# Performance work log

Measured on AMD Instinct MI355X. Metric: run time of the kernel, lower is better.

The kernel has to match this reference:

```python
import jax, jax.numpy as jnp
import numpy as np

B, L, D = 32, 4096, 64
TOP_K = 2
KS = 25            # AvgPool1d kernel_size
PAD = (KS - 1) // 2
LN_EPS = 1e-5


def setup_inputs() -> dict:
    key = jax.random.key(0)
    ks = jax.random.split(key, 8)
    s = lambda fan_in: 1.0 / np.sqrt(fan_in)
    return {
        "x": jax.random.normal(ks[0], (B, L, 1), dtype=jnp.float32),
        "embed_w": jax.random.normal(ks[1], (1, D), dtype=jnp.float32) * s(1),
        "embed_b": jnp.zeros((D,), jnp.float32),
        "q_w": jax.random.normal(ks[2], (D, D), dtype=jnp.float32) * s(D),
        "q_b": jnp.zeros((D,), jnp.float32),
        "k_w": jax.random.normal(ks[3], (D, D), dtype=jnp.float32) * s(D),
        "k_b": jnp.zeros((D,), jnp.float32),
        "v_w": jax.random.normal(ks[4], (D, D), dtype=jnp.float32) * s(D),
        "v_b": jnp.zeros((D,), jnp.float32),
        "ln_g": jnp.ones((D,), jnp.float32),
        "ln_b": jnp.zeros((D,), jnp.float32),
        "fc_w": jax.random.normal(ks[5], (L * D, 1), dtype=jnp.float32) * s(L * D),
        "fc_b": jnp.zeros((1,), jnp.float32),
    }


def _auto_correlation(h, q_w, q_b, k_w, k_b, v_w, v_b):
    Q = h @ q_w + q_b          # (B, L, D)
    K = h @ k_w + k_b
    V = h @ v_w + v_b
    q_fft = jnp.fft.rfft(Q, axis=1)
    k_fft = jnp.fft.rfft(K, axis=1)
    corr = jnp.fft.irfft(q_fft * jnp.conj(k_fft), n=L, axis=1)  # (B, L, D)
    mean_corr = corr.mean(axis=-1)                               # (B, L)
    topk_vals, topk_idx = jax.lax.top_k(mean_corr, TOP_K)        # (B, K)
    weights = jax.nn.softmax(topk_vals, axis=-1)                 # (B, K)
    # torch.roll(V[b], shift=lag): out[i] = V[(i - lag) mod L]
    idx = (jnp.arange(L)[None, None, :] - topk_idx[:, :, None]) % L   # (B, K, L)
    Vg = jnp.take_along_axis(V[:, None, :, :], idx[..., None], axis=2)  # (B, K, L, D)
    return jnp.einsum("bk,bkld->bld", weights, Vg)


def _moving_avg(h):
    # AvgPool1d(kernel=KS, stride=1, pad=PAD, count_include_pad=True) over time axis
    hp = jnp.pad(h, ((0, 0), (PAD, PAD), (0, 0)))
    cs = jnp.pad(jnp.cumsum(hp, axis=1), ((0, 0), (1, 0), (0, 0)))
    return (cs[:, KS:, :] - cs[:, :-KS, :]) / KS   # (B, L, D)


def reference(x, embed_w, embed_b, q_w, q_b, k_w, k_b, v_w, v_b,
              ln_g, ln_b, fc_w, fc_b):
    h = x @ embed_w + embed_b                       # (B, L, D)
    ac = _auto_correlation(h, q_w, q_b, k_w, k_b, v_w, v_b)
    z = h + ac
    mu = z.mean(axis=-1, keepdims=True)
    var = z.var(axis=-1, keepdims=True)
    hn = (z - mu) * jax.lax.rsqrt(var + LN_EPS) * ln_g + ln_b
    trend = _moving_avg(hn)
    seasonal = hn - trend
    return seasonal.reshape(B, L * D) @ fc_w + fc_b  # (B, 1)
```

## Files before the change

### kernel.cpp

```cpp
#include <hip/hip_runtime.h>
#include <math.h>

#define LQ 4096
#define DQ 64
#define BQ 32
#define KSQ 25
#define PADQ 12
#define LN_EPS 1e-5f

#define NT 8
#define TCH (LQ / NT)

#define WS_U    16
#define WS_V    80
#define WS_W    144
#define WS_F    256
#define WS_TOP  (WS_F + 4 * LQ)
#define WS_PART (WS_TOP + BQ * 4)

__device__ __forceinline__ float wave_sum64(float v) {
    for (int o = 32; o > 0; o >>= 1) v += __shfl_xor(v, o, 64);
    return v;
}

__global__ void ac_prep_kernel(const float* __restrict__ embed_w,
                               const float* __restrict__ embed_b,
                               const float* __restrict__ q_w, const float* __restrict__ q_b,
                               const float* __restrict__ k_w, const float* __restrict__ k_b,
                               const float* __restrict__ v_w, const float* __restrict__ v_b,
                               const float* __restrict__ ln_g,
                               float* __restrict__ ws) {
    int d = threadIdx.x;
    float Aq = 0.f, Cq = 0.f, Ak = 0.f, Ck = 0.f, Av = 0.f, Cv = 0.f;
#pragma unroll 8
    for (int e = 0; e < DQ; ++e) {
        float we = embed_w[e], be = embed_b[e];
        float qw = q_w[e * DQ + d], kw = k_w[e * DQ + d], vw = v_w[e * DQ + d];
        Aq = fmaf(we, qw, Aq); Cq = fmaf(be, qw, Cq);
        Ak = fmaf(we, kw, Ak); Ck = fmaf(be, kw, Ck);
        Av = fmaf(we, vw, Av); Cv = fmaf(be, vw, Cv);
    }
    Cq += q_b[d]; Ck += k_b[d]; Cv += v_b[d];

    float cx = embed_w[d];
    float cs = Av;
    float cc = embed_b[d] + Cv;

    const float invD = 1.f / (float)DQ;
    float mx = wave_sum64(cx) * invD;
    float ms = wave_sum64(cs) * invD;
    float mc = wave_sum64(cc) * invD;
    float cxp = cx - mx, csp = cs - ms, ccp = cc - mc;

    float Mxx = wave_sum64(cxp * cxp) * invD;
    float Mss = wave_sum64(csp * csp) * invD;
    float Mcc = wave_sum64(ccp * ccp) * invD;
    float Mxs = wave_sum64(cxp * csp) * invD;
    float Mxc = wave_sum64(cxp * ccp) * invD;
    float Msc = wave_sum64(csp * ccp) * invD;

    float alpha = wave_sum64(Aq * Ak) * invD;
    float beta  = wave_sum64(Aq * Ck + Ak * Cq) * invD;
    float gamma = wave_sum64(Cq * Ck) * ((float)LQ * invD);

    float g = ln_g[d];
    ws[WS_U + d] = cxp * g;
    ws[WS_V + d] = csp * g;
    ws[WS_W + d] = ccp * g;
    if (d == 0) {
        ws[0] = alpha; ws[1] = beta; ws[2] = gamma;
        ws[3] = Mxx; ws[4] = Mss; ws[5] = Mcc;
        ws[6] = Mxs; ws[7] = Mxc; ws[8] = Msc;
    }
}

__global__ void ac_prepF_kernel(const float* __restrict__ fc_w,
                                const float* __restrict__ ln_b,
                                float* __restrict__ ws) {
    __shared__ float su[DQ], sv[DQ], sw[DQ], sb[DQ];
    if (threadIdx.x < DQ) {
        su[threadIdx.x] = ws[WS_U + threadIdx.x];
        sv[threadIdx.x] = ws[WS_V + threadIdx.x];
        sw[threadIdx.x] = ws[WS_W + threadIdx.x];
        sb[threadIdx.x] = ln_b[threadIdx.x];
    }
    __syncthreads();
    int l = blockIdx.x * 256 + threadIdx.x;
    const float4* fc = (const float4*)(fc_w + (size_t)l * DQ);
    float fu = 0.f, fv = 0.f, fw = 0.f, fb = 0.f;
#pragma unroll
    for (int d4 = 0; d4 < DQ / 4; ++d4) {
        float4 f = fc[d4];
        int d = d4 * 4;
        fu = fmaf(su[d], f.x, fu); fu = fmaf(su[d+1], f.y, fu); fu = fmaf(su[d+2], f.z, fu); fu = fmaf(su[d+3], f.w, fu);
        fv = fmaf(sv[d], f.x, fv); fv = fmaf(sv[d+1], f.y, fv); fv = fmaf(sv[d+2], f.z, fv); fv = fmaf(sv[d+3], f.w, fv);
        fw = fmaf(sw[d], f.x, fw); fw = fmaf(sw[d+1], f.y, fw); fw = fmaf(sw[d+2], f.z, fw); fw = fmaf(sw[d+3], f.w, fw);
        fb = fmaf(sb[d], f.x, fb); fb = fmaf(sb[d+1], f.y, fb); fb = fmaf(sb[d+2], f.z, fb); fb = fmaf(sb[d+3], f.w, fb);
    }
    ws[WS_F + l]          = fu;
    ws[WS_F + LQ + l]     = fv;
    ws[WS_F + 2 * LQ + l] = fw;
    ws[WS_F + 3 * LQ + l] = fb;
}

__global__ void ac_autocorr_kernel(const float* __restrict__ x,
                                   float* __restrict__ ws) {
    __shared__ float sA[TCH];
    __shared__ float sB[TCH + 1024];
    int b = blockIdx.x;
    int lagbase = blockIdx.y << 10;
    int t0 = blockIdx.z * TCH;
    const float* xb = x + (size_t)b * LQ;
    int tid = threadIdx.x;

    for (int i = tid; i < TCH; i += 256) sA[i] = xb[t0 + i];
    int start = t0 - lagbase - 1023;
    for (int j = tid; j < TCH + 1024; j += 256)
        sB[j] = xb[(start + j + LQ) & (LQ - 1)];
    __syncthreads();

    const float4* sA4 = (const float4*)sA;
    const float4* sB4 = (const float4*)sB;
    int base = 255 - tid;
    float4 w0 = sB4[base];
    float a0 = 0.f, a1 = 0.f, a2 = 0.f, a3 = 0.f;
#pragma unroll 4
    for (int c = 0; c < TCH / 4; ++c) {
        float4 w1 = sB4[base + c + 1];
        float4 xa = sA4[c];
        a0 = fmaf(xa.x, w0.w, a0); a1 = fmaf(xa.x, w0.z, a1); a2 = fmaf(xa.x, w0.y, a2); a3 = fmaf(xa.x, w0.x, a3);
        a0 = fmaf(xa.y, w1.x, a0); a1 = fmaf(xa.y, w0.w, a1); a2 = fmaf(xa.y, w0.z, a2); a3 = fmaf(xa.y, w0.y, a3);
        a0 = fmaf(xa.z, w1.y, a0); a1 = fmaf(xa.z, w1.x, a1); a2 = fmaf(xa.z, w0.w, a2); a3 = fmaf(xa.z, w0.z, a3);
        a0 = fmaf(xa.w, w1.z, a0); a1 = fmaf(xa.w, w1.y, a1); a2 = fmaf(xa.w, w1.x, a2); a3 = fmaf(xa.w, w0.w, a3);
        w0 = w1;
    }
    float4* part4 = (float4*)(ws + WS_PART);
    part4[((size_t)(blockIdx.z * BQ + b) * 512) + (blockIdx.y * 256) + tid] =
        make_float4(a0, a1, a2, a3);
}

__device__ __forceinline__ bool ac_better(float v, int i, float v2, int i2) {
    return (v > v2) || (v == v2 && i < i2);
}
__global__ void ac_top2_kernel(const float* __restrict__ x,
                               float* __restrict__ ws) {
    __shared__ float sred[256], rred[256];
    __shared__ float sv0[256], sv1[256];
    __shared__ int   si0[256], si1[256];
    int b = blockIdx.x;
    int tid = threadIdx.x;
    const float* xb = x + (size_t)b * LQ;

    float sx = 0.f, r2k = 0.f;
    for (int t = tid; t < LQ; t += 256) {
        float v = xb[t];
        sx  += v;
        r2k += v * xb[(t + 2048) & (LQ - 1)];
    }
    sred[tid] = sx; rred[tid] = r2k;
    __syncthreads();
    for (int st = 128; st > 0; st >>= 1) {
        if (tid < st) { sred[tid] += sred[tid + st]; rred[tid] += rred[tid + st]; }
        __syncthreads();
    }
    float Sx = sred[0], R2048 = rred[0];
    float alpha = ws[0], beta = ws[1], gamma = ws[2];
    float cbase = fmaf(beta, Sx, gamma);

    float v0 = -3.0e38f, v1 = -3.0e38f;
    int i0 = 1 << 30, i1 = 1 << 30;
    const float* part = ws + WS_PART;
    for (int lag = tid; lag < 2048; lag += 256) {
        float R = 0.f;
#pragma unroll
        for (int z = 0; z < NT; ++z)
            R += part[((size_t)(z * BQ + b) * 2048) + lag];
        float v = fmaf(alpha, R, cbase);
        if (ac_better(v, lag, v0, i0)) { v1 = v0; i1 = i0; v0 = v; i0 = lag; }
        else if (ac_better(v, lag, v1, i1)) { v1 = v; i1 = lag; }
        int mir = (LQ - lag) & (LQ - 1);
        if (mir != lag) {
            if (ac_better(v, mir, v0, i0)) { v1 = v0; i1 = i0; v0 = v; i0 = mir; }
            else if (ac_better(v, mir, v1, i1)) { v1 = v; i1 = mir; }
        }
    }
    if (tid == 0) {
        float v = fmaf(alpha, R2048, cbase);
        if (ac_better(v, 2048, v0, i0)) { v1 = v0; i1 = i0; v0 = v; i0 = 2048; }
        else if (ac_better(v, 2048, v1, i1)) { v1 = v; i1 = 2048; }
    }
    sv0[tid] = v0; sv1[tid] = v1; si0[tid] = i0; si1[tid] = i1;
    __syncthreads();
    for (int st = 128; st > 0; st >>= 1) {
        if (tid < st) {
            float a0 = sv0[tid], a1 = sv1[tid];
            int   c0 = si0[tid], c1 = si1[tid];
            float u0 = sv0[tid + st], u1 = sv1[tid + st];
            int   j0 = si0[tid + st], j1 = si1[tid + st];
            float t0v, t1v; int t0i, t1i;
            if (ac_better(a0, c0, u0, j0)) {
                t0v = a0; t0i = c0;
                if (ac_better(u0, j0, a1, c1)) { t1v = u0; t1i = j0; } else { t1v = a1; t1i = c1; }
            } else {
                t0v = u0; t0i = j0;
                if (ac_better(a0, c0, u1, j1)) { t1v = a0; t1i = c0; } else { t1v = u1; t1i = j1; }
            }
            sv0[tid] = t0v; si0[tid] = t0i;
            sv1[tid] = t1v; si1[tid] = t1i;
        }
        __syncthreads();
    }
    if (tid == 0) {
        float w0 = 1.f / (1.f + expf(sv1[0] - sv0[0]));
        float* top = ws + WS_TOP + b * 4;
        top[0] = (float)si0[0]; top[1] = (float)si1[0];
        top[2] = w0; top[3] = 1.f - w0;
    }
}

__global__ void ac_final_kernel(const float* __restrict__ x,
                                const float* __restrict__ fc_b,
                                const float* __restrict__ ws,
                                float* __restrict__ out) {
    __shared__ float pL[LQ], qL[LQ], rL[LQ];
    __shared__ float wred[16];
    int b = blockIdx.x;
    int tid = threadIdx.x;
    const float* xb = x + (size_t)b * LQ;
    const float* top = ws + WS_TOP + b * 4;
    int lag0 = (int)top[0], lag1 = (int)top[1];
    float w0 = top[2], w1 = top[3];
    float Mxx = ws[3], Mss = ws[4], Mcc = ws[5], Mxs = ws[6], Mxc = ws[7], Msc = ws[8];

    for (int l = tid; l < LQ; l += 1024) {
        float xv = xb[l];
        float xs = w0 * xb[(l - lag0) & (LQ - 1)] + w1 * xb[(l - lag1) & (LQ - 1)];
        float var = xv * xv * Mxx + xs * xs * Mss + Mcc
                  + 2.f * xv * xs * Mxs + 2.f * xv * Mxc + 2.f * xs * Msc;
        float r = rsqrtf(var + LN_EPS);
        pL[l] = xv * r; qL[l] = xs * r; rL[l] = r;
    }
    __syncthreads();

    const float* Fu = ws + WS_F;
    const float* Fv = Fu + LQ;
    const float* Fw = Fv + LQ;
    const float* FB = Fw + LQ;
    const float inv = 1.f / (float)KSQ;
    float acc = 0.f;
    for (int l = tid; l < LQ; l += 1024) {
        int lo = l - PADQ; if (lo < 0) lo = 0;
        int hi = l + PADQ; if (hi > LQ - 1) hi = LQ - 1;
        float sp = 0.f, sq = 0.f, sr = 0.f;
        for (int j = lo; j <= hi; ++j) { sp += pL[j]; sq += qL[j]; sr += rL[j]; }
        float cnt = (float)(hi - lo + 1);
        acc += (pL[l] - sp * inv) * Fu[l]
             + (qL[l] - sq * inv) * Fv[l]
             + (rL[l] - sr * inv) * Fw[l]
             + (1.f - cnt * inv) * FB[l];
    }
    acc = wave_sum64(acc);
    int wid = tid >> 6;
    if ((tid & 63) == 0) wred[wid] = acc;
    __syncthreads();
    if (tid == 0) {
        float s = 0.f;
#pragma unroll
        for (int w = 0; w < 16; ++w) s += wred[w];
        out[b] = s + fc_b[0];
    }
}

extern "C" void kernel_launch(void* const* d_in, const int* in_sizes, int n_in,
                              void* d_out, int out_size, void* d_ws, size_t ws_size,
                              hipStream_t stream) {
    const float* x       = (const float*)d_in[0];
    const float* embed_w = (const float*)d_in[1];
    const float* embed_b = (const float*)d_in[2];
    const float* q_w     = (const float*)d_in[3];
    const float* q_b     = (const float*)d_in[4];
    const float* k_w     = (const float*)d_in[5];
    const float* k_b     = (const float*)d_in[6];
    const float* v_w     = (const float*)d_in[7];
    const float* v_b     = (const float*)d_in[8];
    const float* ln_g    = (const float*)d_in[9];
    const float* ln_b    = (const float*)d_in[10];
    const float* fc_w    = (const float*)d_in[11];
    const float* fc_b    = (const float*)d_in[12];
    float* out = (float*)d_out;
    float* ws  = (float*)d_ws;

    ac_prep_kernel<<<1, 64, 0, stream>>>(embed_w, embed_b, q_w, q_b, k_w, k_b,
                                         v_w, v_b, ln_g, ws);
    ac_prepF_kernel<<<16, 256, 0, stream>>>(fc_w, ln_b, ws);
    ac_autocorr_kernel<<<dim3(BQ, 2, NT), 256, 0, stream>>>(x, ws);
    ac_top2_kernel<<<BQ, 256, 0, stream>>>(x, ws);
    ac_final_kernel<<<BQ, 1024, 0, stream>>>(x, fc_b, ws, out);
}
```

Measured before the change: 128.4 us.

## Fuse five kernels into two and move moving-average onto fc weights

Merges the parameter prep, fc-weight projection and autocorrelation partial sums into one heterogeneous launch, and folds top-2 selection into the final kernel with wave-shuffle reductions. The moving-average subtraction is moved algebraically onto the projected fc weights (the pool is applied to the F vectors instead of the per-batch normalized signals), removing the 25-tap windowed loop per batch. This cuts launch count and per-batch work, at the cost of every final block redundantly recomputing the small prep scalars.

New measurement: 116.6 us. 9.2% less time.

```diff
diff --git a/kernel.cpp b/kernel.cpp
--- a/kernel.cpp
+++ b/kernel.cpp
@@ -10,263 +10,306 @@
 
 #define NT 8
 #define TCH (LQ / NT)
-
-#define WS_U    16
-#define WS_V    80
-#define WS_W    144
-#define WS_F    256
-#define WS_TOP  (WS_F + 4 * LQ)
-#define WS_PART (WS_TOP + BQ * 4)
+#define NAC (BQ * 2 * NT)
+
+#define WS_PART 16384
 
 __device__ __forceinline__ float wave_sum64(float v) {
     for (int o = 32; o > 0; o >>= 1) v += __shfl_xor(v, o, 64);
     return v;
 }
 
-__global__ void ac_prep_kernel(const float* __restrict__ embed_w,
-                               const float* __restrict__ embed_b,
-                               const float* __restrict__ q_w, const float* __restrict__ q_b,
-                               const float* __restrict__ k_w, const float* __restrict__ k_b,
-                               const float* __restrict__ v_w, const float* __restrict__ v_b,
-                               const float* __restrict__ ln_g,
-                               float* __restrict__ ws) {
-    int d = threadIdx.x;
-    float Aq = 0.f, Cq = 0.f, Ak = 0.f, Ck = 0.f, Av = 0.f, Cv = 0.f;
-#pragma unroll 8
-    for (int e = 0; e < DQ; ++e) {
-        float we = embed_w[e], be = embed_b[e];
-        float qw = q_w[e * DQ + d], kw = k_w[e * DQ + d], vw = v_w[e * DQ + d];
-        Aq = fmaf(we, qw, Aq); Cq = fmaf(be, qw, Cq);
-        Ak = fmaf(we, kw, Ak); Ck = fmaf(be, kw, Ck);
-        Av = fmaf(we, vw, Av); Cv = fmaf(be, vw, Cv);
-    }
-    Cq += q_b[d]; Ck += k_b[d]; Cv += v_b[d];
-
-    float cx = embed_w[d];
-    float cs = Av;
-    float cc = embed_b[d] + Cv;
-
-    const float invD = 1.f / (float)DQ;
-    float mx = wave_sum64(cx) * invD;
-    float ms = wave_sum64(cs) * invD;
-    float mc = wave_sum64(cc) * invD;
-    float cxp = cx - mx, csp = cs - ms, ccp = cc - mc;
-
-    float Mxx = wave_sum64(cxp * cxp) * invD;
-    float Mss = wave_sum64(csp * csp) * invD;
-    float Mcc = wave_sum64(ccp * ccp) * invD;
-    float Mxs = wave_sum64(cxp * csp) * invD;
-    float Mxc = wave_sum64(cxp * ccp) * invD;
-    float Msc = wave_sum64(csp * ccp) * invD;
-
-    float alpha = wave_sum64(Aq * Ak) * invD;
-    float beta  = wave_sum64(Aq * Ck + Ak * Cq) * invD;
-    float gamma = wave_sum64(Cq * Ck) * ((float)LQ * invD);
-
-    float g = ln_g[d];
-    ws[WS_U + d] = cxp * g;
-    ws[WS_V + d] = csp * g;
-    ws[WS_W + d] = ccp * g;
-    if (d == 0) {
-        ws[0] = alpha; ws[1] = beta; ws[2] = gamma;
-        ws[3] = Mxx; ws[4] = Mss; ws[5] = Mcc;
-        ws[6] = Mxs; ws[7] = Mxc; ws[8] = Msc;
-    }
-}
-
-__global__ void ac_prepF_kernel(const float* __restrict__ fc_w,
-                                const float* __restrict__ ln_b,
-                                float* __restrict__ ws) {
-    __shared__ float su[DQ], sv[DQ], sw[DQ], sb[DQ];
-    if (threadIdx.x < DQ) {
-        su[threadIdx.x] = ws[WS_U + threadIdx.x];
-        sv[threadIdx.x] = ws[WS_V + threadIdx.x];
-        sw[threadIdx.x] = ws[WS_W + threadIdx.x];
-        sb[threadIdx.x] = ln_b[threadIdx.x];
-    }
-    __syncthreads();
-    int l = blockIdx.x * 256 + threadIdx.x;
-    const float4* fc = (const float4*)(fc_w + (size_t)l * DQ);
-    float fu = 0.f, fv = 0.f, fw = 0.f, fb = 0.f;
-#pragma unroll
-    for (int d4 = 0; d4 < DQ / 4; ++d4) {
-        float4 f = fc[d4];
-        int d = d4 * 4;
-        fu = fmaf(su[d], f.x, fu); fu = fmaf(su[d+1], f.y, fu); fu = fmaf(su[d+2], f.z, fu); fu = fmaf(su[d+3], f.w, fu);
-        fv = fmaf(sv[d], f.x, fv); fv = fmaf(sv[d+1], f.y, fv); fv = fmaf(sv[d+2], f.z, fv); fv = fmaf(sv[d+3], f.w, fv);
-        fw = fmaf(sw[d], f.x, fw); fw = fmaf(sw[d+1], f.y, fw); fw = fmaf(sw[d+2], f.z, fw); fw = fmaf(sw[d+3], f.w, fw);
-        fb = fmaf(sb[d], f.x, fb); fb = fmaf(sb[d+1], f.y, fb); fb = fmaf(sb[d+2], f.z, fb); fb = fmaf(sb[d+3], f.w, fb);
-    }
-    ws[WS_F + l]          = fu;
-    ws[WS_F + LQ + l]     = fv;
-    ws[WS_F + 2 * LQ + l] = fw;
-    ws[WS_F + 3 * LQ + l] = fb;
-}
-
-__global__ void ac_autocorr_kernel(const float* __restrict__ x,
-                                   float* __restrict__ ws) {
-    __shared__ float sA[TCH];
-    __shared__ float sB[TCH + 1024];
-    int b = blockIdx.x;
-    int lagbase = blockIdx.y << 10;
-    int t0 = blockIdx.z * TCH;
-    const float* xb = x + (size_t)b * LQ;
-    int tid = threadIdx.x;
-
-    for (int i = tid; i < TCH; i += 256) sA[i] = xb[t0 + i];
-    int start = t0 - lagbase - 1023;
-    for (int j = tid; j < TCH + 1024; j += 256)
-        sB[j] = xb[(start + j + LQ) & (LQ - 1)];
-    __syncthreads();
-
-    const float4* sA4 = (const float4*)sA;
-    const float4* sB4 = (const float4*)sB;
-    int base = 255 - tid;
-    float4 w0 = sB4[base];
-    float a0 = 0.f, a1 = 0.f, a2 = 0.f, a3 = 0.f;
-#pragma unroll 4
-    for (int c = 0; c < TCH / 4; ++c) {
-        float4 w1 = sB4[base + c + 1];
-        float4 xa = sA4[c];
-        a0 = fmaf(xa.x, w0.w, a0); a1 = fmaf(xa.x, w0.z, a1); a2 = fmaf(xa.x, w0.y, a2); a3 = fmaf(xa.x, w0.x, a3);
-        a0 = fmaf(xa.y, w1.x, a0); a1 = fmaf(xa.y, w0.w, a1); a2 = fmaf(xa.y, w0.z, a2); a3 = fmaf(xa.y, w0.y, a3);
-        a0 = fmaf(xa.z, w1.y, a0); a1 = fmaf(xa.z, w1.x, a1); a2 = fmaf(xa.z, w0.w, a2); a3 = fmaf(xa.z, w0.z, a3);
-        a0 = fmaf(xa.w, w1.z, a0); a1 = fmaf(xa.w, w1.y, a1); a2 = fmaf(xa.w, w1.x, a2); a3 = fmaf(xa.w, w0.w, a3);
-        w0 = w1;
-    }
-    float4* part4 = (float4*)(ws + WS_PART);
-    part4[((size_t)(blockIdx.z * BQ + b) * 512) + (blockIdx.y * 256) + tid] =
-        make_float4(a0, a1, a2, a3);
-}
-
 __device__ __forceinline__ bool ac_better(float v, int i, float v2, int i2) {
     return (v > v2) || (v == v2 && i < i2);
 }
-__global__ void ac_top2_kernel(const float* __restrict__ x,
-                               float* __restrict__ ws) {
-    __shared__ float sred[256], rred[256];
-    __shared__ float sv0[256], sv1[256];
-    __shared__ int   si0[256], si1[256];
+
+__global__ void ac_stage1_kernel(const float* __restrict__ x,
+                                 const float* __restrict__ fc_w,
+                                 const float* __restrict__ ln_g,
+                                 const float* __restrict__ ln_b,
+                                 const float* __restrict__ embed_w,
+                                 const float* __restrict__ embed_b,
+                                 const float* __restrict__ v_w,
+                                 const float* __restrict__ v_b,
+                                 float* __restrict__ ws) {
+    __shared__ float smem[2048];
+    int tid = threadIdx.x;
+
+    if (blockIdx.x < NAC) {
+        float* sA = smem;
+        float* sB = smem + TCH;
+        int b = blockIdx.x & 31;
+        int y = (blockIdx.x >> 5) & 1;
+        int z = blockIdx.x >> 6;
+        int lagbase = y << 10;
+        int t0 = z * TCH;
+        const float* xb = x + (size_t)b * LQ;
+
+        for (int i = tid; i < TCH; i += 256) sA[i] = xb[t0 + i];
+        int start = t0 - lagbase - 1023;
+        for (int j = tid; j < TCH + 1024; j += 256)
+            sB[j] = xb[(start + j + LQ) & (LQ - 1)];
+        __syncthreads();
+
+        const float4* sA4 = (const float4*)sA;
+        const float4* sB4 = (const float4*)sB;
+        int base = 255 - tid;
+        float4 w0 = sB4[base];
+        float a0 = 0.f, a1 = 0.f, a2 = 0.f, a3 = 0.f;
+#pragma unroll 4
+        for (int c = 0; c < TCH / 4; ++c) {
+            float4 w1 = sB4[base + c + 1];
+            float4 xa = sA4[c];
+            a0 = fmaf(xa.x, w0.w, a0); a1 = fmaf(xa.x, w0.z, a1); a2 = fmaf(xa.x, w0.y, a2); a3 = fmaf(xa.x, w0.x, a3);
+            a0 = fmaf(xa.y, w1.x, a0); a1 = fmaf(xa.y, w0.w, a1); a2 = fmaf(xa.y, w0.z, a2); a3 = fmaf(xa.y, w0.y, a3);
+            a0 = fmaf(xa.z, w1.y, a0); a1 = fmaf(xa.z, w1.x, a1); a2 = fmaf(xa.z, w0.w, a2); a3 = fmaf(xa.z, w0.z, a3);
+            a0 = fmaf(xa.w, w1.z, a0); a1 = fmaf(xa.w, w1.y, a1); a2 = fmaf(xa.w, w1.x, a2); a3 = fmaf(xa.w, w0.w, a3);
+            w0 = w1;
+        }
+        float4* part4 = (float4*)(ws + WS_PART);
+        part4[((size_t)(z * BQ + b) * 512) + (y * 256) + tid] =
+            make_float4(a0, a1, a2, a3);
+    } else {
+        float* Hu = smem;
+        float* Hv = smem + 280;
+        float* Hw = smem + 560;
+        float* Hb = smem + 840;
+        float* su = smem + 1120;
+        float* sv = smem + 1184;
+        float* sw = smem + 1248;
+        float* sb = smem + 1312;
+
+        if (tid < DQ) {
+            int d = tid;
+            float Av = 0.f, Cv = 0.f;
+#pragma unroll 8
+            for (int e = 0; e < DQ; ++e) {
+                float vw = v_w[e * DQ + d];
+                Av = fmaf(embed_w[e], vw, Av);
+                Cv = fmaf(embed_b[e], vw, Cv);
+            }
+            Cv += v_b[d];
+            float cx = embed_w[d];
+            float cs = Av;
+            float cc = embed_b[d] + Cv;
+            const float invD = 1.f / (float)DQ;
+            float mx = wave_sum64(cx) * invD;
+            float ms = wave_sum64(cs) * invD;
+            float mc = wave_sum64(cc) * invD;
+            float g = ln_g[d];
+            su[d] = (cx - mx) * g;
+            sv[d] = (cs - ms) * g;
+            sw[d] = (cc - mc) * g;
+            sb[d] = ln_b[d];
+        }
+        __syncthreads();
+
+        int lbase = (blockIdx.x - NAC) * 256;
+        for (int i = tid; i < 256 + 2 * PADQ; i += 256) {
+            int l = lbase - PADQ + i;
+            float fu = 0.f, fv = 0.f, fw = 0.f, fb = 0.f;
+            if (l >= 0 && l < LQ) {
+                const float4* fc = (const float4*)(fc_w + (size_t)l * DQ);
+#pragma unroll
+                for (int d4 = 0; d4 < DQ / 4; ++d4) {
+                    float4 f = fc[d4];
+                    int d = d4 * 4;
+                    fu = fmaf(su[d], f.x, fu); fu = fmaf(su[d+1], f.y, fu); fu = fmaf(su[d+2], f.z, fu); fu = fmaf(su[d+3], f.w, fu);
+                    fv = fmaf(sv[d], f.x, fv); fv = fmaf(sv[d+1], f.y, fv); fv = fmaf(sv[d+2], f.z, fv); fv = fmaf(sv[d+3], f.w, fv);
+                    fw = fmaf(sw[d], f.x, fw); fw = fmaf(sw[d+1], f.y, fw); fw = fmaf(sw[d+2], f.z, fw); fw = fmaf(sw[d+3], f.w, fw);
+                    fb = fmaf(sb[d], f.x, fb); fb = fmaf(sb[d+1], f.y, fb); fb = fmaf(sb[d+2], f.z, fb); fb = fmaf(sb[d+3], f.w, fb);
+                }
+            }
+            Hu[i] = fu; Hv[i] = fv; Hw[i] = fw; Hb[i] = fb;
+        }
+        __syncthreads();
+
+        int l = lbase + tid;
+        int i = tid + PADQ;
+        float Gu = 0.f, Gv = 0.f, Gw = 0.f;
+#pragma unroll
+        for (int k = -PADQ; k <= PADQ; ++k) {
+            Gu += Hu[i + k]; Gv += Hv[i + k]; Gw += Hw[i + k];
+        }
+        int lo = l - PADQ; if (lo < 0) lo = 0;
+        int hi = l + PADQ; if (hi > LQ - 1) hi = LQ - 1;
+        const float inv = 1.f / (float)KSQ;
+        float cnt = (float)(hi - lo + 1);
+        ws[l]          = Hu[i] - Gu * inv;
+        ws[LQ + l]     = Hv[i] - Gv * inv;
+        ws[2 * LQ + l] = Hw[i] - Gw * inv;
+        ws[3 * LQ + l] = (1.f - cnt * inv) * Hb[i];
+    }
+}
+
+__global__ void __launch_bounds__(1024)
+ac_final_kernel(const float* __restrict__ x,
+                const float* __restrict__ embed_w, const float* __restrict__ embed_b,
+                const float* __restrict__ q_w, const float* __restrict__ q_b,
+                const float* __restrict__ k_w, const float* __restrict__ k_b,
+                const float* __restrict__ v_w, const float* __restrict__ v_b,
+                const float* __restrict__ fc_b,
+                const float* __restrict__ ws,
+                float* __restrict__ out) {
+    __shared__ float4 xs4_[LQ / 4];
+    __shared__ float scal[16];
+    __shared__ float red[32];
+    __shared__ float tv0[16], tv1[16];
+    __shared__ int   ti0[16], ti1[16];
+    float* xs_ = (float*)xs4_;
+
     int b = blockIdx.x;
     int tid = threadIdx.x;
+    int wv = tid >> 6;
     const float* xb = x + (size_t)b * LQ;
 
-    float sx = 0.f, r2k = 0.f;
-    for (int t = tid; t < LQ; t += 256) {
-        float v = xb[t];
-        sx  += v;
-        r2k += v * xb[(t + 2048) & (LQ - 1)];
-    }
-    sred[tid] = sx; rred[tid] = r2k;
-    __syncthreads();
-    for (int st = 128; st > 0; st >>= 1) {
-        if (tid < st) { sred[tid] += sred[tid + st]; rred[tid] += rred[tid + st]; }
-        __syncthreads();
-    }
-    float Sx = sred[0], R2048 = rred[0];
-    float alpha = ws[0], beta = ws[1], gamma = ws[2];
-    float cbase = fmaf(beta, Sx, gamma);
-
-    float v0 = -3.0e38f, v1 = -3.0e38f;
-    int i0 = 1 << 30, i1 = 1 << 30;
-    const float* part = ws + WS_PART;
-    for (int lag = tid; lag < 2048; lag += 256) {
-        float R = 0.f;
-#pragma unroll
-        for (int z = 0; z < NT; ++z)
-            R += part[((size_t)(z * BQ + b) * 2048) + lag];
-        float v = fmaf(alpha, R, cbase);
-        if (ac_better(v, lag, v0, i0)) { v1 = v0; i1 = i0; v0 = v; i0 = lag; }
-        else if (ac_better(v, lag, v1, i1)) { v1 = v; i1 = lag; }
-        int mir = (LQ - lag) & (LQ - 1);
-        if (mir != lag) {
-            if (ac_better(v, mir, v0, i0)) { v1 = v0; i1 = i0; v0 = v; i0 = mir; }
-            else if (ac_better(v, mir, v1, i1)) { v1 = v; i1 = mir; }
-        }
-    }
+    xs4_[tid] = ((const float4*)xb)[tid];
+
+    if (tid < DQ) {
+        int d = tid;
+        float Aq = 0.f, Cq = 0.f, Ak = 0.f, Ck = 0.f, Av = 0.f, Cv = 0.f;
+#pragma unroll 8
+        for (int e = 0; e < DQ; ++e) {
+            float we = embed_w[e], be = embed_b[e];
+            float qw = q_w[e * DQ + d], kw = k_w[e * DQ + d], vw = v_w[e * DQ + d];
+            Aq = fmaf(we, qw, Aq); Cq = fmaf(be, qw, Cq);
+            Ak = fmaf(we, kw, Ak); Ck = fmaf(be, kw, Ck);
+            Av = fmaf(we, vw, Av); Cv = fmaf(be, vw, Cv);
+        }
+        Cq += q_b[d]; Ck += k_b[d]; Cv += v_b[d];
+        float cx = embed_w[d];
+        float cs = Av;
+        float cc = embed_b[d] + Cv;
+        const float invD = 1.f / (float)DQ;
+        float mx = wave_sum64(cx) * invD;
+        float ms = wave_sum64(cs) * invD;
+        float mc = wave_sum64(cc) * invD;
+        float cxp = cx - mx, csp = cs - ms, ccp = cc - mc;
+        float Mxx = wave_sum64(cxp * cxp) * invD;
+        float Mss = wave_sum64(csp * csp) * invD;
+        float Mcc = wave_sum64(ccp * ccp) * invD;
+        float Mxs = wave_sum64(cxp * csp) * invD;
+        float Mxc = wave_sum64(cxp * ccp) * invD;
+        float Msc = wave_sum64(csp * ccp) * invD;
+        float alpha = wave_sum64(Aq * Ak) * invD;
+        float beta  = wave_sum64(Aq * Ck + Ak * Cq) * invD;
+        float gamma = wave_sum64(Cq * Ck) * ((float)LQ * invD);
+        if (d == 0) {
+            scal[2] = alpha; scal[3] = beta; scal[4] = gamma;
+            scal[5] = Mxx; scal[6] = Mss; scal[7] = Mcc;
+            scal[8] = Mxs; scal[9] = Mxc; scal[10] = Msc;
+        }
+    }
+    __syncthreads();
+
+    {
+        float sx = 0.f, r2k = 0.f;
+#pragma unroll
+        for (int k = 0; k < 4; ++k) {
+            int t = tid + k * 1024;
+            float v = xs_[t];
+            sx  += v;
+            r2k += v * xs_[(t + 2048) & (LQ - 1)];
+        }
+        sx  = wave_sum64(sx);
+        r2k = wave_sum64(r2k);
+        if ((tid & 63) == 0) { red[wv] = sx; red[16 + wv] = r2k; }
+    }
+    __syncthreads();
     if (tid == 0) {
-        float v = fmaf(alpha, R2048, cbase);
-        if (ac_better(v, 2048, v0, i0)) { v1 = v0; i1 = i0; v0 = v; i0 = 2048; }
-        else if (ac_better(v, 2048, v1, i1)) { v1 = v; i1 = 2048; }
-    }
-    sv0[tid] = v0; sv1[tid] = v1; si0[tid] = i0; si1[tid] = i1;
-    __syncthreads();
-    for (int st = 128; st > 0; st >>= 1) {
-        if (tid < st) {
-            float a0 = sv0[tid], a1 = sv1[tid];
-            int   c0 = si0[tid], c1 = si1[tid];
-            float u0 = sv0[tid + st], u1 = sv1[tid + st];
-            int   j0 = si0[tid + st], j1 = si1[tid + st];
-            float t0v, t1v; int t0i, t1i;
-            if (ac_better(a0, c0, u0, j0)) {
-                t0v = a0; t0i = c0;
-                if (ac_better(u0, j0, a1, c1)) { t1v = u0; t1i = j0; } else { t1v = a1; t1i = c1; }
-            } else {
-                t0v = u0; t0i = j0;
-                if (ac_better(a0, c0, u1, j1)) { t1v = a0; t1i = c0; } else { t1v = u1; t1i = j1; }
+        float sx = 0.f, r2k = 0.f;
+#pragma unroll
+        for (int w = 0; w < 16; ++w) { sx += red[w]; r2k += red[16 + w]; }
+        scal[0] = sx; scal[1] = r2k;
+        scal[11] = fmaf(scal[3], sx, scal[4]);
+    }
+    __syncthreads();
+
+    {
+        float alpha = scal[2], cbase = scal[11];
+        float v0 = -3.0e38f, v1 = -3.0e38f;
+        int i0 = 1 << 30, i1 = 1 << 30;
+        const float* part = ws + WS_PART;
+#pragma unroll
+        for (int k = 0; k < 2; ++k) {
+            int lag = tid + k * 1024;
+            float R = 0.f;
+#pragma unroll
+            for (int z = 0; z < NT; ++z)
+                R += part[((size_t)(z * BQ + b) * 2048) + lag];
+            float v = fmaf(alpha, R, cbase);
+            if (ac_better(v, lag, v0, i0)) { v1 = v0; i1 = i0; v0 = v; i0 = lag; }
+            else if (ac_better(v, lag, v1, i1)) { v1 = v; i1 = lag; }
+            int mir = (LQ - lag) & (LQ - 1);
+            if (mir != lag) {
+                if (ac_better(v, mir, v0, i0)) { v1 = v0; i1 = i0; v0 = v; i0 = mir; }
+                else if (ac_better(v, mir, v1, i1)) { v1 = v; i1 = mir; }
             }
-            sv0[tid] = t0v; si0[tid] = t0i;
-            sv1[tid] = t1v; si1[tid] = t1i;
-        }
-        __syncthreads();
-    }
+        }
+        for (int o = 32; o > 0; o >>= 1) {
+            float u0 = __shfl_xor(v0, o, 64); int j0 = __shfl_xor(i0, o, 64);
+            float u1 = __shfl_xor(v1, o, 64); int j1 = __shfl_xor(i1, o, 64);
+            if (ac_better(u0, j0, v0, i0)) {
+                if (ac_better(v0, i0, u1, j1)) { v1 = v0; i1 = i0; }
+                else                           { v1 = u1; i1 = j1; }
+                v0 = u0; i0 = j0;
+            } else if (ac_better(u0, j0, v1, i1)) { v1 = u0; i1 = j0; }
+        }
+        if ((tid & 63) == 0) { tv0[wv] = v0; ti0[wv] = i0; tv1[wv] = v1; ti1[wv] = i1; }
+    }
+    __syncthreads();
     if (tid == 0) {
-        float w0 = 1.f / (1.f + expf(sv1[0] - sv0[0]));
-        float* top = ws + WS_TOP + b * 4;
-        top[0] = (float)si0[0]; top[1] = (float)si1[0];
-        top[2] = w0; top[3] = 1.f - w0;
-    }
-}
-
-__global__ void ac_final_kernel(const float* __restrict__ x,
-                                const float* __restrict__ fc_b,
-                                const float* __restrict__ ws,
-                                float* __restrict__ out) {
-    __shared__ float pL[LQ], qL[LQ], rL[LQ];
-    __shared__ float wred[16];
-    int b = blockIdx.x;
-    int tid = threadIdx.x;
-    const float* xb = x + (size_t)b * LQ;
-    const float* top = ws + WS_TOP + b * 4;
-    int lag0 = (int)top[0], lag1 = (int)top[1];
-    float w0 = top[2], w1 = top[3];
-    float Mxx = ws[3], Mss = ws[4], Mcc = ws[5], Mxs = ws[6], Mxc = ws[7], Msc = ws[8];
-
-    for (int l = tid; l < LQ; l += 1024) {
-        float xv = xb[l];
-        float xs = w0 * xb[(l - lag0) & (LQ - 1)] + w1 * xb[(l - lag1) & (LQ - 1)];
-        float var = xv * xv * Mxx + xs * xs * Mss + Mcc
-                  + 2.f * xv * xs * Mxs + 2.f * xv * Mxc + 2.f * xs * Msc;
-        float r = rsqrtf(var + LN_EPS);
-        pL[l] = xv * r; qL[l] = xs * r; rL[l] = r;
-    }
-    __syncthreads();
-
-    const float* Fu = ws + WS_F;
-    const float* Fv = Fu + LQ;
-    const float* Fw = Fv + LQ;
-    const float* FB = Fw + LQ;
-    const float inv = 1.f / (float)KSQ;
-    float acc = 0.f;
-    for (int l = tid; l < LQ; l += 1024) {
-        int lo = l - PADQ; if (lo < 0) lo = 0;
-        int hi = l + PADQ; if (hi > LQ - 1) hi = LQ - 1;
-        float sp = 0.f, sq = 0.f, sr = 0.f;
-        for (int j = lo; j <= hi; ++j) { sp += pL[j]; sq += qL[j]; sr += rL[j]; }
-        float cnt = (float)(hi - lo + 1);
-        acc += (pL[l] - sp * inv) * Fu[l]
-             + (qL[l] - sq * inv) * Fv[l]
-             + (rL[l] - sr * inv) * Fw[l]
-             + (1.f - cnt * inv) * FB[l];
-    }
-    acc = wave_sum64(acc);
-    int wid = tid >> 6;
-    if ((tid & 63) == 0) wred[wid] = acc;
+        float v0 = tv0[0], v1 = tv1[0];
+        int i0 = ti0[0], i1 = ti1[0];
+#pragma unroll
+        for (int w = 1; w < 16; ++w) {
+            float u0 = tv0[w], u1 = tv1[w];
+            int j0 = ti0[w], j1 = ti1[w];
+            if (ac_better(u0, j0, v0, i0)) {
+                if (ac_better(v0, i0, u1, j1)) { v1 = v0; i1 = i0; }
+                else                           { v1 = u1; i1 = j1; }
+                v0 = u0; i0 = j0;
+            } else if (ac_better(u0, j0, v1, i1)) { v1 = u0; i1 = j0; }
+        }
+        float v2k = fmaf(scal[2], scal[1], scal[11]);
+        if (ac_better(v2k, 2048, v0, i0)) {
+            if (ac_better(v0, i0, v1, i1)) { v1 = v0; i1 = i0; }
+            v0 = v2k; i0 = 2048;
+        } else if (ac_better(v2k, 2048, v1, i1)) { v1 = v2k; i1 = 2048; }
+        float w0 = 1.f / (1.f + expf(v1 - v0));
+        scal[12] = (float)i0; scal[13] = (float)i1;
+        scal[14] = w0; scal[15] = 1.f - w0;
+    }
+    __syncthreads();
+
+    {
+        int lag0 = (int)scal[12], lag1 = (int)scal[13];
+        float w0 = scal[14], w1 = scal[15];
+        float Mxx = scal[5], Mss = scal[6], Mcc = scal[7];
+        float Mxs = scal[8], Mxc = scal[9], Msc = scal[10];
+        const float* Fpu = ws;
+        const float* Fpv = ws + LQ;
+        const float* Fpw = ws + 2 * LQ;
+        const float* FBp = ws + 3 * LQ;
+        float acc = 0.f;
+#pragma unroll
+        for (int k = 0; k < 4; ++k) {
+            int l = tid + k * 1024;
+            float xv = xs_[l];
+            float xsv = w0 * xs_[(l - lag0) & (LQ - 1)] + w1 * xs_[(l - lag1) & (LQ - 1)];
+            float var = xv * xv * Mxx + xsv * xsv * Mss + Mcc
+                      + 2.f * xv * xsv * Mxs + 2.f * xv * Mxc + 2.f * xsv * Msc;
+            float r = rsqrtf(var + LN_EPS);
+            acc += (xv * r) * Fpu[l] + (xsv * r) * Fpv[l] + r * Fpw[l] + FBp[l];
+        }
+        acc = wave_sum64(acc);
+        if ((tid & 63) == 0) red[wv] = acc;
+    }
     __syncthreads();
     if (tid == 0) {
         float s = 0.f;
 #pragma unroll
-        for (int w = 0; w < 16; ++w) s += wred[w];
+        for (int w = 0; w < 16; ++w) s += red[w];
         out[b] = s + fc_b[0];
     }
 }
@@ -290,10 +333,8 @@
     float* out = (float*)d_out;
     float* ws  = (float*)d_ws;
 
-    ac_prep_kernel<<<1, 64, 0, stream>>>(embed_w, embed_b, q_w, q_b, k_w, k_b,
-                                         v_w, v_b, ln_g, ws);
-    ac_prepF_kernel<<<16, 256, 0, stream>>>(fc_w, ln_b, ws);
-    ac_autocorr_kernel<<<dim3(BQ, 2, NT), 256, 0, stream>>>(x, ws);
-    ac_top2_kernel<<<BQ, 256, 0, stream>>>(x, ws);
-    ac_final_kernel<<<BQ, 1024, 0, stream>>>(x, fc_b, ws, out);
-}
+    ac_stage1_kernel<<<NAC + 16, 256, 0, stream>>>(x, fc_w, ln_g, ln_b,
+                                                   embed_w, embed_b, v_w, v_b, ws);
+    ac_final_kernel<<<BQ, 1024, 0, stream>>>(x, embed_w, embed_b, q_w, q_b,
+                                             k_w, k_b, v_w, v_b, fc_b, ws, out);
+}
```
